# Kernel optimization log

Hardware: AMD Instinct MI355X
Metric: run time of the kernel (lower is better)

The kernel has to match this reference:

```python
import jax, jax.numpy as jnp
import numpy as np

BATCH = 16384
CLASS_NUM = 2048
TEMPERATURE = 1.0
EPS = 1e-8


def _neg_mask_flat_indices(N):
    # Static mask: all pairs except diagonal and the (i, i+C)/(i+C, i) positives.
    C = N // 2
    mask = np.ones((N, N), dtype=bool)
    np.fill_diagonal(mask, False)
    i = np.arange(C)
    mask[i, i + C] = False
    mask[i + C, i] = False
    return np.flatnonzero(mask.reshape(-1))  # [N * (N - 2)]


_NEG_IDX = _neg_mask_flat_indices(2 * CLASS_NUM)


def setup_inputs() -> dict:
    key = jax.random.key(0)
    k1, k2 = jax.random.split(key)
    q_i = jax.random.uniform(k1, (BATCH, CLASS_NUM), dtype=jnp.float32)
    q_j = jax.random.uniform(k2, (BATCH, CLASS_NUM), dtype=jnp.float32)
    return {"q_i": q_i, "q_j": q_j}


def reference(q_i, q_j):
    C = q_i.shape[1]
    N = 2 * C

    # Entropy regularizer on cluster marginals.
    p_i = q_i.sum(0)
    p_i = p_i / p_i.sum()
    ne_i = jnp.log(jnp.float32(C)) + (p_i * jnp.log(p_i)).sum()
    p_j = q_j.sum(0)
    p_j = p_j / p_j.sum()
    ne_j = jnp.log(jnp.float32(C)) + (p_j * jnp.log(p_j)).sum()
    entropy = ne_i + ne_j

    # Pairwise cosine similarity over cluster columns: q is [N, B].
    q = jnp.concatenate([q_i.T, q_j.T], axis=0)
    norms = jnp.linalg.norm(q, axis=1)  # [N]
    sim = (q @ q.T) / jnp.maximum(norms[:, None] * norms[None, :], EPS)
    sim = sim / TEMPERATURE

    # Positives: off-diagonals at +/- C.
    pos = jnp.concatenate([jnp.diagonal(sim, C), jnp.diagonal(sim, -C)])[:, None]  # [N, 1]
    # Negatives: static masked gather, N-2 per row.
    neg = sim.reshape(-1)[_NEG_IDX].reshape(N, N - 2)

    logits = jnp.concatenate([pos, neg], axis=1)  # [N, N-1], label = 0
    # CrossEntropyLoss(reduction='sum') with all labels == 0, then / N.
    ce = (jax.nn.logsumexp(logits, axis=1) - logits[:, 0]).sum() / N
    return ce + entropy
```

## Files before the change

kernel.cpp:

```cpp
#include <hip/hip_runtime.h>
#include <hip/hip_bf16.h>
#include <cstdint>
#include <cstddef>

#define KDIM  16384
#define CNUM  2048
#define NROW  4096
#define BM    256
#define BK    32
#define NT    (KDIM / BK)

typedef __attribute__((ext_vector_type(8))) short bf16x8;
typedef __attribute__((ext_vector_type(4))) float f32x4;

__global__ __launch_bounds__(256) void transpose_sums_kernel(
    const float* __restrict__ qi, const float* __restrict__ qj,
    ushort* __restrict__ Qbf, float* __restrict__ p, float* __restrict__ sq)
{
    __shared__ float tile[64][68];
    const int tid = threadIdx.x;
    const int tt  = blockIdx.x;
    const int at  = blockIdx.y;
    const int t0  = tt * 64;
    const float* src = (at < 32) ? qi : qj;
    const int c0 = (at < 32 ? at : at - 32) * 64;

    {
        const int tl = tid >> 2;
        const int cl = (tid & 3) * 16;
        const float* s = src + (size_t)(t0 + tl) * CNUM + c0 + cl;
        float4 v0 = *(const float4*)(s);
        float4 v1 = *(const float4*)(s + 4);
        float4 v2 = *(const float4*)(s + 8);
        float4 v3 = *(const float4*)(s + 12);
        *(float4*)&tile[tl][cl]      = v0;
        *(float4*)&tile[tl][cl + 4]  = v1;
        *(float4*)&tile[tl][cl + 8]  = v2;
        *(float4*)&tile[tl][cl + 12] = v3;
    }
    __syncthreads();

    const int al   = tid >> 2;
    const int tseg = tid & 3;
    float s1 = 0.f, s2 = 0.f;
    ushort outv[16] __attribute__((aligned(16)));
#pragma unroll
    for (int k = 0; k < 16; ++k) {
        float v = tile[tseg * 16 + k][al];
        s1 += v; s2 += v * v;
        __hip_bfloat16 h = __float2bfloat16(v);
        outv[k] = *(ushort*)&h;
    }
    const size_t dst = (size_t)(at * 64 + al) * KDIM + t0 + tseg * 16;
    *(uint4*)(Qbf + dst)     = *(uint4*)&outv[0];
    *(uint4*)(Qbf + dst + 8) = *(uint4*)&outv[8];

    s1 += __shfl_xor(s1, 1); s1 += __shfl_xor(s1, 2);
    s2 += __shfl_xor(s2, 1); s2 += __shfl_xor(s2, 2);
    if (tseg == 0) {
        atomicAdd(&p[at * 64 + al], s1);
        atomicAdd(&sq[at * 64 + al], s2);
    }
}

__global__ void rnorm_kernel(const float* __restrict__ sq, float* __restrict__ rnorm)
{
    int a = blockIdx.x * 256 + threadIdx.x;
    if (a < NROW) rnorm[a] = 1.0f / sqrtf(fmaxf(sq[a], 1e-30f));
}

__global__ __launch_bounds__(512) void gram_lse_kernel(
    const ushort* __restrict__ Q, const float* __restrict__ rnorm,
    float* __restrict__ pM, float* __restrict__ pS, float* __restrict__ pos)
{
    __shared__ ushort lds[2][2][BM][BK];

    const int tid  = threadIdx.x;
    const int lane = tid & 63;
    const int wid  = tid >> 6;
    const int wr   = wid >> 2;
    const int wc   = wid & 3;
    const int g    = lane >> 4;
    const int c15  = lane & 15;
    const int I = blockIdx.y, J = blockIdx.x;
    const int Ibase = I * BM, Jbase = J * BM;

    const int srow = tid >> 2;
    const int skk  = (tid & 3) * 8;
    const ushort* gA0 = Q + (size_t)(Ibase + srow) * KDIM + skk;
    const ushort* gA1 = Q + (size_t)(Ibase + 128 + srow) * KDIM + skk;
    const ushort* gB0 = Q + (size_t)(Jbase + srow) * KDIM + skk;
    const ushort* gB1 = Q + (size_t)(Jbase + 128 + srow) * KDIM + skk;

    auto stage = [&](int buf, int kt) {
        const int k0 = kt * BK;
        __builtin_amdgcn_global_load_lds(
            (const __attribute__((address_space(1))) void*)(gA0 + k0),
            (__attribute__((address_space(3))) void*)&lds[buf][0][wid * 16][0],
            16, 0, 0);
        __builtin_amdgcn_global_load_lds(
            (const __attribute__((address_space(1))) void*)(gA1 + k0),
            (__attribute__((address_space(3))) void*)&lds[buf][0][128 + wid * 16][0],
            16, 0, 0);
        __builtin_amdgcn_global_load_lds(
            (const __attribute__((address_space(1))) void*)(gB0 + k0),
            (__attribute__((address_space(3))) void*)&lds[buf][1][wid * 16][0],
            16, 0, 0);
        __builtin_amdgcn_global_load_lds(
            (const __attribute__((address_space(1))) void*)(gB1 + k0),
            (__attribute__((address_space(3))) void*)&lds[buf][1][128 + wid * 16][0],
            16, 0, 0);
    };

    f32x4 acc[8][4] = {};

    stage(0, 0);
    __syncthreads();
    int cur = 0;
    for (int kt = 0; kt < NT; ++kt) {
        if (kt + 1 < NT) stage(cur ^ 1, kt + 1);
        bf16x8 bfr[4], af[8];
#pragma unroll
        for (int n = 0; n < 4; ++n)
            bfr[n] = *(const bf16x8*)&lds[cur][1][wc * 64 + n * 16 + c15][g * 8];
#pragma unroll
        for (int m = 0; m < 8; ++m)
            af[m] = *(const bf16x8*)&lds[cur][0][wr * 128 + m * 16 + c15][g * 8];
#pragma unroll
        for (int m = 0; m < 8; ++m)
#pragma unroll
            for (int n = 0; n < 4; ++n)
                acc[m][n] = __builtin_amdgcn_mfma_f32_16x16x32_bf16(af[m], bfr[n], acc[m][n], 0, 0, 0);
        __syncthreads();
        cur ^= 1;
    }

    float rb[4], ra[8][4];
#pragma unroll
    for (int n = 0; n < 4; ++n) rb[n] = rnorm[Jbase + wc * 64 + n * 16 + c15];
#pragma unroll
    for (int m = 0; m < 8; ++m)
#pragma unroll
        for (int r = 0; r < 4; ++r)
            ra[m][r] = rnorm[Ibase + wr * 128 + m * 16 + g * 4 + r];

    const bool diagT = (I == J);
    const bool posT  = (J == (I ^ 8));
#pragma unroll
    for (int m = 0; m < 8; ++m) {
#pragma unroll
        for (int n = 0; n < 4; ++n) {
#pragma unroll
            for (int r = 0; r < 4; ++r) {
                float sv = acc[m][n][r] * ra[m][r] * rb[n];
                const int aoff = wr * 128 + m * 16 + g * 4 + r;
                const int boff = wc * 64 + n * 16 + c15;
                if (posT && aoff == boff) pos[Ibase + aoff] = sv;
                if (diagT && aoff == boff) sv = -1e30f;
                acc[m][n][r] = sv;
            }
        }
    }

#pragma unroll
    for (int m = 0; m < 8; ++m) {
#pragma unroll
        for (int r = 0; r < 4; ++r) {
            float mx = fmaxf(fmaxf(acc[m][0][r], acc[m][1][r]),
                             fmaxf(acc[m][2][r], acc[m][3][r]));
#pragma unroll
            for (int d = 8; d >= 1; d >>= 1) mx = fmaxf(mx, __shfl_xor(mx, d));
            float s = 0.f;
#pragma unroll
            for (int n = 0; n < 4; ++n) s += __expf(acc[m][n][r] - mx);
#pragma unroll
            for (int d = 8; d >= 1; d >>= 1) s += __shfl_xor(s, d);
            if (c15 == 0) {
                const int a  = Ibase + wr * 128 + m * 16 + g * 4 + r;
                const int Jc = J * 4 + wc;
                pM[(size_t)Jc * NROW + a] = mx;
                pS[(size_t)Jc * NROW + a] = s;
            }
        }
    }
}

__global__ __launch_bounds__(256) void combine_kernel(
    const float* __restrict__ pM, const float* __restrict__ pS,
    const float* __restrict__ pos, float* __restrict__ ce_acc)
{
    const int a = blockIdx.x * 256 + threadIdx.x;
    float mx = -1e30f;
#pragma unroll 8
    for (int j = 0; j < 64; ++j) mx = fmaxf(mx, pM[(size_t)j * NROW + a]);
    float s = 0.f;
#pragma unroll 8
    for (int j = 0; j < 64; ++j)
        s += pS[(size_t)j * NROW + a] * __expf(pM[(size_t)j * NROW + a] - mx);
    float ce = mx + logf(s) - pos[a];

    float v = ce;
#pragma unroll
    for (int d = 32; d >= 1; d >>= 1) v += __shfl_xor(v, d);
    __shared__ float red[4];
    if ((threadIdx.x & 63) == 0) red[threadIdx.x >> 6] = v;
    __syncthreads();
    if (threadIdx.x == 0)
        atomicAdd(ce_acc, red[0] + red[1] + red[2] + red[3]);
}

__global__ __launch_bounds__(256) void finalize_kernel(
    const float* __restrict__ p, const float* __restrict__ ce_acc,
    float* __restrict__ out)
{
    const int tid = threadIdx.x;
    float spi = 0.f, spli = 0.f, spj = 0.f, splj = 0.f;
    for (int c = tid; c < CNUM; c += 256) {
        float v = p[c];        spi += v; spli += v * logf(v);
        float w = p[CNUM + c]; spj += w; splj += w * logf(w);
    }
#pragma unroll
    for (int d = 32; d >= 1; d >>= 1) {
        spi  += __shfl_xor(spi, d);  spli += __shfl_xor(spli, d);
        spj  += __shfl_xor(spj, d);  splj += __shfl_xor(splj, d);
    }
    __shared__ float r4[4][4];
    if ((tid & 63) == 0) {
        int w = tid >> 6;
        r4[w][0] = spi; r4[w][1] = spli; r4[w][2] = spj; r4[w][3] = splj;
    }
    __syncthreads();
    if (tid == 0) {
        spi  = r4[0][0] + r4[1][0] + r4[2][0] + r4[3][0];
        spli = r4[0][1] + r4[1][1] + r4[2][1] + r4[3][1];
        spj  = r4[0][2] + r4[1][2] + r4[2][2] + r4[3][2];
        splj = r4[0][3] + r4[1][3] + r4[2][3] + r4[3][3];
        float nei = logf((float)CNUM) + spli / spi - logf(spi);
        float nej = logf((float)CNUM) + splj / spj - logf(spj);
        out[0] = ce_acc[0] / (float)NROW + nei + nej;
    }
}

extern "C" void kernel_launch(void* const* d_in, const int* in_sizes, int n_in,
                              void* d_out, int out_size, void* d_ws, size_t ws_size,
                              hipStream_t stream)
{
    const float* qi = (const float*)d_in[0];
    const float* qj = (const float*)d_in[1];
    float* out = (float*)d_out;

    char* ws = (char*)d_ws;
    const size_t QB = (size_t)NROW * KDIM * sizeof(ushort);
    ushort* Qbf  = (ushort*)ws;
    float* p     = (float*)(ws + QB);
    float* sq    = (float*)(ws + QB + 16384);
    float* ce    = (float*)(ws + QB + 32768);
    float* rnorm = (float*)(ws + QB + 33024);
    float* pos   = (float*)(ws + QB + 49408);
    float* pM    = (float*)(ws + QB + 65792);
    float* pS    = (float*)(ws + QB + 65792 + 1048576);

    hipMemsetAsync(ws + QB, 0, 33024, stream);

    dim3 gT(256, 64);
    transpose_sums_kernel<<<gT, 256, 0, stream>>>(qi, qj, Qbf, p, sq);
    rnorm_kernel<<<16, 256, 0, stream>>>(sq, rnorm);
    dim3 gG(16, 16);
    gram_lse_kernel<<<gG, 512, 0, stream>>>(Qbf, rnorm, pM, pS, pos);
    combine_kernel<<<16, 256, 0, stream>>>(pM, pS, pos, ce);
    finalize_kernel<<<1, 256, 0, stream>>>(p, ce, out);
}
```

Before: 816.8 us.

## Double GEMM K-tile to 64 with XOR-swizzled LDS layout

Doubles the K depth of each staged tile in the Gram GEMM, which halves the number of barrier-separated iterations. The LDS layout moves to dynamic shared memory with an XOR swizzle on the 16-byte segments so the fragment reads avoid bank conflicts. LDS use per block grows to 128 KB, which may limit occupancy to one block per CU, and the launch now needs a dynamic shared-memory attribute call on every invocation.

```diff
diff --git a/kernel.cpp b/kernel.cpp
--- a/kernel.cpp
+++ b/kernel.cpp
@@ -7,7 +7,7 @@
 #define CNUM  2048
 #define NROW  4096
 #define BM    256
-#define BK    32
+#define BK    64
 #define NT    (KDIM / BK)
 
 typedef __attribute__((ext_vector_type(8))) short bf16x8;
@@ -73,7 +73,7 @@
     const ushort* __restrict__ Q, const float* __restrict__ rnorm,
     float* __restrict__ pM, float* __restrict__ pS, float* __restrict__ pos)
 {
-    __shared__ ushort lds[2][2][BM][BK];
+    extern __shared__ ushort L[];
 
     const int tid  = threadIdx.x;
     const int lane = tid & 63;
@@ -85,31 +85,30 @@
     const int I = blockIdx.y, J = blockIdx.x;
     const int Ibase = I * BM, Jbase = J * BM;
 
-    const int srow = tid >> 2;
-    const int skk  = (tid & 3) * 8;
-    const ushort* gA0 = Q + (size_t)(Ibase + srow) * KDIM + skk;
-    const ushort* gA1 = Q + (size_t)(Ibase + 128 + srow) * KDIM + skk;
-    const ushort* gB0 = Q + (size_t)(Jbase + srow) * KDIM + skk;
-    const ushort* gB1 = Q + (size_t)(Jbase + 128 + srow) * KDIM + skk;
+    const int r8 = lane >> 3;
+    const int sseg = (lane & 7) ^ r8;
+    const ushort* gA[4];
+    const ushort* gB[4];
+#pragma unroll
+    for (int q = 0; q < 4; ++q) {
+        const int row = q * 64 + wid * 8 + r8;
+        gA[q] = Q + (size_t)(Ibase + row) * KDIM + sseg * 8;
+        gB[q] = Q + (size_t)(Jbase + row) * KDIM + sseg * 8;
+    }
 
     auto stage = [&](int buf, int kt) {
         const int k0 = kt * BK;
-        __builtin_amdgcn_global_load_lds(
-            (const __attribute__((address_space(1))) void*)(gA0 + k0),
-            (__attribute__((address_space(3))) void*)&lds[buf][0][wid * 16][0],
-            16, 0, 0);
-        __builtin_amdgcn_global_load_lds(
-            (const __attribute__((address_space(1))) void*)(gA1 + k0),
-            (__attribute__((address_space(3))) void*)&lds[buf][0][128 + wid * 16][0],
-            16, 0, 0);
-        __builtin_amdgcn_global_load_lds(
-            (const __attribute__((address_space(1))) void*)(gB0 + k0),
-            (__attribute__((address_space(3))) void*)&lds[buf][1][wid * 16][0],
-            16, 0, 0);
-        __builtin_amdgcn_global_load_lds(
-            (const __attribute__((address_space(1))) void*)(gB1 + k0),
-            (__attribute__((address_space(3))) void*)&lds[buf][1][128 + wid * 16][0],
-            16, 0, 0);
+#pragma unroll
+        for (int q = 0; q < 4; ++q) {
+            __builtin_amdgcn_global_load_lds(
+                (const __attribute__((address_space(1))) void*)(gA[q] + k0),
+                (__attribute__((address_space(3))) void*)&L[((buf * 2 + 0) * 256 + q * 64 + wid * 8) * 64],
+                16, 0, 0);
+            __builtin_amdgcn_global_load_lds(
+                (const __attribute__((address_space(1))) void*)(gB[q] + k0),
+                (__attribute__((address_space(3))) void*)&L[((buf * 2 + 1) * 256 + q * 64 + wid * 8) * 64],
+                16, 0, 0);
+        }
     };
 
     f32x4 acc[8][4] = {};
@@ -119,18 +118,22 @@
     int cur = 0;
     for (int kt = 0; kt < NT; ++kt) {
         if (kt + 1 < NT) stage(cur ^ 1, kt + 1);
-        bf16x8 bfr[4], af[8];
-#pragma unroll
-        for (int n = 0; n < 4; ++n)
-            bfr[n] = *(const bf16x8*)&lds[cur][1][wc * 64 + n * 16 + c15][g * 8];
-#pragma unroll
-        for (int m = 0; m < 8; ++m)
-            af[m] = *(const bf16x8*)&lds[cur][0][wr * 128 + m * 16 + c15][g * 8];
-#pragma unroll
-        for (int m = 0; m < 8; ++m)
+#pragma unroll
+        for (int kh = 0; kh < 2; ++kh) {
+            const int slot = ((kh << 2) | g) ^ (c15 & 7);
+            bf16x8 bfr[4], af[8];
 #pragma unroll
             for (int n = 0; n < 4; ++n)
-                acc[m][n] = __builtin_amdgcn_mfma_f32_16x16x32_bf16(af[m], bfr[n], acc[m][n], 0, 0, 0);
+                bfr[n] = *(const bf16x8*)&L[((cur * 2 + 1) * 256 + wc * 64 + n * 16 + c15) * 64 + slot * 8];
+#pragma unroll
+            for (int m = 0; m < 8; ++m)
+                af[m] = *(const bf16x8*)&L[((cur * 2 + 0) * 256 + wr * 128 + m * 16 + c15) * 64 + slot * 8];
+#pragma unroll
+            for (int m = 0; m < 8; ++m)
+#pragma unroll
+                for (int n = 0; n < 4; ++n)
+                    acc[m][n] = __builtin_amdgcn_mfma_f32_16x16x32_bf16(af[m], bfr[n], acc[m][n], 0, 0, 0);
+        }
         __syncthreads();
         cur ^= 1;
     }
@@ -260,13 +263,16 @@
     float* pM    = (float*)(ws + QB + 65792);
     float* pS    = (float*)(ws + QB + 65792 + 1048576);
 
+    hipFuncSetAttribute((const void*)gram_lse_kernel,
+                        hipFuncAttributeMaxDynamicSharedMemorySize, 131072);
+
     hipMemsetAsync(ws + QB, 0, 33024, stream);
 
     dim3 gT(256, 64);
     transpose_sums_kernel<<<gT, 256, 0, stream>>>(qi, qj, Qbf, p, sq);
     rnorm_kernel<<<16, 256, 0, stream>>>(sq, rnorm);
     dim3 gG(16, 16);
-    gram_lse_kernel<<<gG, 512, 0, stream>>>(Qbf, rnorm, pM, pS, pos);
+    gram_lse_kernel<<<gG, 512, 131072, stream>>>(Qbf, rnorm, pM, pS, pos);
     combine_kernel<<<16, 256, 0, stream>>>(pM, pS, pos, ce);
     finalize_kernel<<<1, 256, 0, stream>>>(p, ce, out);
 }
```

Measured after the change: 726.7 us. 1.12x faster.
